# Kernel optimization log

Hardware: AMD Instinct MI355X
Metric: run time of the kernel (lower is better)

## Reference

```python
import jax, jax.numpy as jnp
import numpy as np

H = 8  # heads

def setup_inputs() -> dict:
    key = jax.random.key(0)
    k0, k1, k2, k3 = jax.random.split(key, 4)
    B, L, D = 4, 1024, 512
    K = jax.random.normal(k0, (B, L, D), dtype=jnp.float32)
    Q = jax.random.normal(k1, (B, L, D), dtype=jnp.float32)
    V = jax.random.normal(k2, (B, L, D), dtype=jnp.float32)
    # realistic padding: each doc has a valid length in [L/2, L]
    lengths = jax.random.randint(k3, (B,), L // 2, L + 1)
    pos = jnp.arange(L)
    valid = pos[None, :] < lengths[:, None]          # [B, L]
    pad_mask = valid[:, :, None] & valid[:, None, :]  # [B, L, L]
    bx_packed = ~valid                                # [B, L] True where padded
    doc_sizes = lengths.astype(jnp.float32)[:, None]  # [B, 1]
    gamma = jnp.ones((H,), dtype=jnp.float32)   # LayerNorm(heads) weight
    beta = jnp.zeros((H,), dtype=jnp.float32)   # LayerNorm(heads) bias
    return {"K": K, "Q": Q, "V": V, "doc_sizes": doc_sizes,
            "gamma": gamma, "beta": beta,
            "pad_mask": pad_mask, "bx_packed": bx_packed}


def reference(K, Q, V, doc_sizes, gamma, beta, pad_mask, bx_packed):
    B, L, D = K.shape
    d = D // H
    split = lambda x: x.reshape(B, L, H, d).transpose(0, 2, 1, 3)  # [B,H,L,d]
    k, q, v = split(K), split(Q), split(V)

    # InnerMatrix: inner-product similarity -> [B,H,L,L]
    cw = jnp.einsum('bhld,bhmd->bhlm', k, q)

    # LayerNorm over heads axis (torch views [B,H,L*L] -> [B,L*L,H], LN over H)
    mu = cw.mean(axis=1, keepdims=True)
    var = cw.var(axis=1, keepdims=True)
    cw = (cw - mu) / jnp.sqrt(var + 1e-5)
    cw = cw * gamma[None, :, None, None] + beta[None, :, None, None]
    # leaky = -1.0 default: float(leaky > 0) == 0, leaky-relu branch is a no-op

    # masked softmax over keys, NaN (fully-masked rows) -> 0
    cw = jnp.where(pad_mask[:, None, :, :], cw, -jnp.inf)
    cw = jax.nn.softmax(cw, axis=-1)
    cw = jnp.where(jnp.isnan(cw), 0.0, cw)

    # aggregated per-token weights: sum over queries, mean over heads -> [B,L]
    w = cw.sum(axis=-2).mean(axis=1)
    w = w / doc_sizes
    w = jnp.where(bx_packed, -jnp.inf, w)
    w = jax.nn.softmax(w, axis=-1)
    w = jnp.where(jnp.isnan(w), 0.0, w)

    # weighted V aggregation, merge heads back -> [B,L,D]
    out = jnp.einsum('bhlm,bhmd->bhld', cw, v)
    out = out.transpose(0, 2, 1, 3).reshape(B, L, D)
    return out, w[..., None]
```

## Files before the change

### kernel.cpp

```cpp
#include <hip/hip_runtime.h>
#include <math.h>

#define L_ 1024
#define D_ 512

typedef _Float16 half8 __attribute__((ext_vector_type(8)));
typedef _Float16 half4v __attribute__((ext_vector_type(4)));
typedef float floatx4 __attribute__((ext_vector_type(4)));

__global__ __launch_bounds__(256) void prep(
    const float* __restrict__ K, const float* __restrict__ Q,
    const float* __restrict__ V,
    _Float16* __restrict__ K16, _Float16* __restrict__ Q16,
    _Float16* __restrict__ Vt)
{
    __shared__ _Float16 tile[64][72];
    const int t = threadIdx.x;
    const int bi = blockIdx.x;
    if (bi < 256) {
        for (int it = 0; it < 16; ++it) {
            size_t f = (size_t)bi * 4096 + it * 256 + t;
            const float4* src; _Float16* dst;
            if (f < 524288) { src = (const float4*)K; dst = K16; }
            else            { src = (const float4*)Q; dst = Q16; f -= 524288; }
            float4 v = src[f];
            half4v h = { (_Float16)v.x, (_Float16)v.y, (_Float16)v.z, (_Float16)v.w };
            *(half4v*)&dst[f * 4] = h;
        }
    } else {
        const int id = bi - 256;
        const int mt = id & 15, h = (id >> 4) & 7, b = id >> 7;
        const float4* Vf4 = (const float4*)V;
        for (int it = 0; it < 4; ++it) {
            const int ml = (t >> 4) + 16 * it;
            const int c4 = t & 15;
            float4 v = Vf4[(size_t)(b * 1024 + mt * 64 + ml) * 128 + h * 16 + c4];
            tile[c4 * 4 + 0][ml] = (_Float16)v.x;
            tile[c4 * 4 + 1][ml] = (_Float16)v.y;
            tile[c4 * 4 + 2][ml] = (_Float16)v.z;
            tile[c4 * 4 + 3][ml] = (_Float16)v.w;
        }
        __syncthreads();
        const int d = t >> 2, seg = t & 3;
        half8 o0 = *(half8*)&tile[d][seg * 16];
        half8 o1 = *(half8*)&tile[d][seg * 16 + 8];
        size_t obase = ((size_t)(b * 8 + h) * 64 + d) * 1024 + mt * 64 + seg * 16;
        *(half8*)&Vt[obase] = o0;
        *(half8*)&Vt[obase + 8] = o1;
    }
}

__global__ __launch_bounds__(256) void qk_ln(
    const _Float16* __restrict__ K16, const _Float16* __restrict__ Q16,
    const float* __restrict__ gamma, const float* __restrict__ beta,
    _Float16* __restrict__ S)
{
    const int t = threadIdx.x;
    const int bi = blockIdx.x;
    const int b = bi & 3;
    const int lt = (bi >> 2) & 63;
    const int ms = bi >> 8;
    const int wv = t >> 6, lane = t & 63;
    const int col = lane & 15, quad = lane >> 4;

    const _Float16* Kb = K16 + (size_t)b * 524288;
    const _Float16* Qb = Q16 + (size_t)b * 524288;
    const size_t krow = (size_t)(lt * 16 + col) * 512;

    float g[8], be[8];
    #pragma unroll
    for (int h = 0; h < 8; ++h) { g[h] = gamma[h]; be[h] = beta[h]; }

    for (int i = 0; i < 4; ++i) {
        const int m0 = (ms * 16 + wv * 4 + i) * 16;
        const size_t qrow = (size_t)(m0 + col) * 512;
        floatx4 c[8];
        #pragma unroll
        for (int h = 0; h < 8; ++h) {
            half8 a0 = *(const half8*)&Kb[krow + h * 64 + quad * 8];
            half8 a1 = *(const half8*)&Kb[krow + h * 64 + 32 + quad * 8];
            half8 b0 = *(const half8*)&Qb[qrow + h * 64 + quad * 8];
            half8 b1 = *(const half8*)&Qb[qrow + h * 64 + 32 + quad * 8];
            floatx4 z = {0.f, 0.f, 0.f, 0.f};
            z    = __builtin_amdgcn_mfma_f32_16x16x32_f16(a0, b0, z, 0, 0, 0);
            c[h] = __builtin_amdgcn_mfma_f32_16x16x32_f16(a1, b1, z, 0, 0, 0);
        }
        #pragma unroll
        for (int r = 0; r < 4; ++r) {
            float mu = 0.f;
            #pragma unroll
            for (int h = 0; h < 8; ++h) mu += c[h][r];
            mu *= 0.125f;
            float var = 0.f;
            #pragma unroll
            for (int h = 0; h < 8; ++h) { float dd = c[h][r] - mu; var += dd * dd; }
            var *= 0.125f;
            const float rs = 1.0f / sqrtf(var + 1e-5f);
            const int l = lt * 16 + quad * 4 + r;
            #pragma unroll
            for (int h = 0; h < 8; ++h) {
                float val = (c[h][r] - mu) * rs * g[h] + be[h];
                S[((size_t)(b * 8 + h) * 1024 + l) * 1024 + m0 + col] = (_Float16)val;
            }
        }
    }
}

__global__ __launch_bounds__(256) void softmax_w(
    _Float16* __restrict__ S, const float* __restrict__ doc,
    float* __restrict__ wacc)
{
    __shared__ float cs[4][1024];
    const int t = threadIdx.x, wv = t >> 6, lane = t & 63;
    const int bi = blockIdx.x;
    const int b = bi & 3, lg = bi >> 2;
    const int len = (int)doc[b];

    float csum[16];
    #pragma unroll
    for (int j = 0; j < 16; ++j) csum[j] = 0.f;

    for (int k = 0; k < 16; ++k) {
        const int rr = wv * 16 + k;
        const int h = rr & 7, li = rr >> 3;
        const int l = lg * 8 + li;
        const size_t base = ((size_t)(b * 8 + h) * 1024 + l) * 1024;
        if (l >= len) {
            half8 z = {};
            *(half8*)&S[base + lane * 8] = z;
            *(half8*)&S[base + 512 + lane * 8] = z;
            continue;
        }
        half8 v1 = *(const half8*)&S[base + lane * 8];
        half8 v2 = *(const half8*)&S[base + 512 + lane * 8];
        float f1[8], f2[8];
        float mx = -INFINITY;
        #pragma unroll
        for (int j = 0; j < 8; ++j) { f1[j] = (float)v1[j]; mx = fmaxf(mx, f1[j]); }
        #pragma unroll
        for (int j = 0; j < 8; ++j) {
            const int m = 512 + lane * 8 + j;
            f2[j] = (m < len) ? (float)v2[j] : -INFINITY;
            mx = fmaxf(mx, f2[j]);
        }
        #pragma unroll
        for (int o = 1; o < 64; o <<= 1) mx = fmaxf(mx, __shfl_xor(mx, o));
        float e1[8], e2[8], sm = 0.f;
        #pragma unroll
        for (int j = 0; j < 8; ++j) { e1[j] = __expf(f1[j] - mx); sm += e1[j]; }
        #pragma unroll
        for (int j = 0; j < 8; ++j) {
            const int m = 512 + lane * 8 + j;
            e2[j] = (m < len) ? __expf(f2[j] - mx) : 0.f;
            sm += e2[j];
        }
        #pragma unroll
        for (int o = 1; o < 64; o <<= 1) sm += __shfl_xor(sm, o);
        const float inv = 1.0f / sm;
        half8 p1, p2;
        #pragma unroll
        for (int j = 0; j < 8; ++j) {
            float q1 = e1[j] * inv, q2 = e2[j] * inv;
            p1[j] = (_Float16)q1; p2[j] = (_Float16)q2;
            csum[j] += q1; csum[8 + j] += q2;
        }
        *(half8*)&S[base + lane * 8] = p1;
        *(half8*)&S[base + 512 + lane * 8] = p2;
    }
    #pragma unroll
    for (int j = 0; j < 8; ++j) {
        cs[wv][lane * 8 + j] = csum[j];
        cs[wv][512 + lane * 8 + j] = csum[8 + j];
    }
    __syncthreads();
    #pragma unroll
    for (int q = 0; q < 4; ++q) {
        const int mm = t + q * 256;
        float s = cs[0][mm] + cs[1][mm] + cs[2][mm] + cs[3][mm];
        atomicAdd(&wacc[b * 1024 + mm], s);
    }
}

__global__ __launch_bounds__(256) void pv(
    const _Float16* __restrict__ P, const _Float16* __restrict__ Vt,
    float* __restrict__ out)
{
    const int t = threadIdx.x, wv = t >> 6, lane = t & 63;
    const int col = lane & 15, quad = lane >> 4;
    const int bi = blockIdx.x;
    const int lb = bi & 15, h = (bi >> 4) & 7, b = bi >> 7;
    const int l0 = lb * 64 + wv * 16;
    const _Float16* Arow = P + ((size_t)(b * 8 + h) * 1024 + l0 + col) * 1024;
    const _Float16* Vb = Vt + (size_t)(b * 8 + h) * 65536;
    floatx4 acc[4] = {{0,0,0,0},{0,0,0,0},{0,0,0,0},{0,0,0,0}};
    for (int kc = 0; kc < 32; ++kc) {
        const int m0 = kc * 32 + quad * 8;
        half8 a = *(const half8*)&Arow[m0];
        #pragma unroll
        for (int dt = 0; dt < 4; ++dt) {
            half8 bf = *(const half8*)&Vb[(size_t)(dt * 16 + col) * 1024 + m0];
            acc[dt] = __builtin_amdgcn_mfma_f32_16x16x32_f16(a, bf, acc[dt], 0, 0, 0);
        }
    }
    #pragma unroll
    for (int r = 0; r < 4; ++r) {
        const int l = l0 + quad * 4 + r;
        float* orow = out + (size_t)(b * 1024 + l) * 512 + h * 64;
        #pragma unroll
        for (int dt = 0; dt < 4; ++dt)
            orow[dt * 16 + col] = acc[dt][r];
    }
}

__global__ __launch_bounds__(256) void w_final(
    const float* __restrict__ wacc, const float* __restrict__ doc,
    float* __restrict__ wout)
{
    const int b = blockIdx.x;
    const int t = threadIdx.x;
    __shared__ float red[4];

    const float ds = doc[b];
    const int len = (int)ds;

    float v[4];
    float mx = -INFINITY;
    #pragma unroll
    for (int i = 0; i < 4; ++i) {
        const int m = t + 256 * i;
        const float raw = wacc[b * L_ + m];
        v[i] = (m < len) ? (raw * 0.125f) / ds : -INFINITY;
        mx = fmaxf(mx, v[i]);
    }
    #pragma unroll
    for (int off = 1; off < 64; off <<= 1) mx = fmaxf(mx, __shfl_xor(mx, off));
    if ((t & 63) == 0) red[t >> 6] = mx;
    __syncthreads();
    mx = fmaxf(fmaxf(red[0], red[1]), fmaxf(red[2], red[3]));

    float e[4];
    float sm = 0.f;
    #pragma unroll
    for (int i = 0; i < 4; ++i) {
        e[i] = (v[i] != -INFINITY) ? __expf(v[i] - mx) : 0.f;
        sm += e[i];
    }
    #pragma unroll
    for (int off = 1; off < 64; off <<= 1) sm += __shfl_xor(sm, off);
    __syncthreads();
    if ((t & 63) == 0) red[t >> 6] = sm;
    __syncthreads();
    sm = red[0] + red[1] + red[2] + red[3];
    const float inv = (sm > 0.f) ? 1.0f / sm : 0.f;

    #pragma unroll
    for (int i = 0; i < 4; ++i)
        wout[b * L_ + t + 256 * i] = e[i] * inv;
}

extern "C" void kernel_launch(void* const* d_in, const int* in_sizes, int n_in,
                              void* d_out, int out_size, void* d_ws, size_t ws_size,
                              hipStream_t stream)
{
    const float* K     = (const float*)d_in[0];
    const float* Q     = (const float*)d_in[1];
    const float* V     = (const float*)d_in[2];
    const float* doc   = (const float*)d_in[3];
    const float* gamma = (const float*)d_in[4];
    const float* beta  = (const float*)d_in[5];

    float* out  = (float*)d_out;
    float* wout = out + (size_t)4 * L_ * D_;

    _Float16* S   = (_Float16*)d_ws;
    _Float16* K16 = S + (size_t)33554432;
    _Float16* Q16 = K16 + 2097152;
    _Float16* Vt  = Q16 + 2097152;
    float*    wacc = (float*)(Vt + 2097152);

    hipMemsetAsync(wacc, 0, 4096 * sizeof(float), stream);
    prep     <<<dim3(768),  dim3(256), 0, stream>>>(K, Q, V, K16, Q16, Vt);
    qk_ln    <<<dim3(1024), dim3(256), 0, stream>>>(K16, Q16, gamma, beta, S);
    softmax_w<<<dim3(512),  dim3(256), 0, stream>>>(S, doc, wacc);
    pv       <<<dim3(512),  dim3(256), 0, stream>>>(S, Vt, out);
    w_final  <<<dim3(4),    dim3(256), 0, stream>>>(wacc, doc, wout);
}
```

Before: 207.9 us.

## Fuse softmax exponent into QK kernel using fixed LayerNorm bound, normalize in PV

```diff
diff --git a/kernel.cpp b/kernel.cpp
--- a/kernel.cpp
+++ b/kernel.cpp
@@ -6,7 +6,10 @@
 
 typedef _Float16 half8 __attribute__((ext_vector_type(8)));
 typedef _Float16 half4v __attribute__((ext_vector_type(4)));
+typedef _Float16 half2v __attribute__((ext_vector_type(2)));
 typedef float floatx4 __attribute__((ext_vector_type(4)));
+
+#define LDS_PITCH 264
 
 __global__ __launch_bounds__(256) void prep(
     const float* __restrict__ K, const float* __restrict__ Q,
@@ -53,40 +56,61 @@
 __global__ __launch_bounds__(256) void qk_ln(
     const _Float16* __restrict__ K16, const _Float16* __restrict__ Q16,
     const float* __restrict__ gamma, const float* __restrict__ beta,
-    _Float16* __restrict__ S)
-{
-    const int t = threadIdx.x;
+    const float* __restrict__ doc,
+    _Float16* __restrict__ S, float* __restrict__ spart)
+{
+    __shared__ _Float16 se[8 * 16 * LDS_PITCH];
+
+    const int t  = threadIdx.x;
     const int bi = blockIdx.x;
-    const int b = bi & 3;
+    const int b  = bi & 3;
     const int lt = (bi >> 2) & 63;
-    const int ms = bi >> 8;
+    const int q  = bi >> 8;
     const int wv = t >> 6, lane = t & 63;
     const int col = lane & 15, quad = lane >> 4;
+    const int len = (int)doc[b];
+    const int lbase = lt * 16;
+
+    float g[8], be[8], M = 0.f;
+    #pragma unroll
+    for (int h = 0; h < 8; ++h) {
+        g[h] = gamma[h]; be[h] = beta[h];
+        M = fmaxf(M, 2.8285f * fabsf(g[h]) + fabsf(be[h]));
+    }
 
     const _Float16* Kb = K16 + (size_t)b * 524288;
     const _Float16* Qb = Q16 + (size_t)b * 524288;
-    const size_t krow = (size_t)(lt * 16 + col) * 512;
-
-    float g[8], be[8];
-    #pragma unroll
-    for (int h = 0; h < 8; ++h) { g[h] = gamma[h]; be[h] = beta[h]; }
-
-    for (int i = 0; i < 4; ++i) {
-        const int m0 = (ms * 16 + wv * 4 + i) * 16;
+    const size_t krow = (size_t)(lbase + col) * 512;
+
+    half8 a0[8], a1[8];
+    #pragma unroll
+    for (int h = 0; h < 8; ++h) {
+        a0[h] = *(const half8*)&Kb[krow + h * 64 + quad * 8];
+        a1[h] = *(const half8*)&Kb[krow + h * 64 + 32 + quad * 8];
+    }
+
+    float sum[8][4];
+    #pragma unroll
+    for (int h = 0; h < 8; ++h)
+        #pragma unroll
+        for (int r = 0; r < 4; ++r) sum[h][r] = 0.f;
+
+    for (int mt = 0; mt < 4; ++mt) {
+        const int m0 = q * 256 + wv * 64 + mt * 16;
         const size_t qrow = (size_t)(m0 + col) * 512;
         floatx4 c[8];
         #pragma unroll
         for (int h = 0; h < 8; ++h) {
-            half8 a0 = *(const half8*)&Kb[krow + h * 64 + quad * 8];
-            half8 a1 = *(const half8*)&Kb[krow + h * 64 + 32 + quad * 8];
             half8 b0 = *(const half8*)&Qb[qrow + h * 64 + quad * 8];
             half8 b1 = *(const half8*)&Qb[qrow + h * 64 + 32 + quad * 8];
             floatx4 z = {0.f, 0.f, 0.f, 0.f};
-            z    = __builtin_amdgcn_mfma_f32_16x16x32_f16(a0, b0, z, 0, 0, 0);
-            c[h] = __builtin_amdgcn_mfma_f32_16x16x32_f16(a1, b1, z, 0, 0, 0);
-        }
+            z    = __builtin_amdgcn_mfma_f32_16x16x32_f16(a0[h], b0, z, 0, 0, 0);
+            c[h] = __builtin_amdgcn_mfma_f32_16x16x32_f16(a1[h], b1, c[h] = z, 0, 0, 0);
+        }
+        const bool mok = (m0 + col) < len;
         #pragma unroll
         for (int r = 0; r < 4; ++r) {
+            const int l = lbase + quad * 4 + r;
             float mu = 0.f;
             #pragma unroll
             for (int h = 0; h < 8; ++h) mu += c[h][r];
@@ -96,106 +120,109 @@
             for (int h = 0; h < 8; ++h) { float dd = c[h][r] - mu; var += dd * dd; }
             var *= 0.125f;
             const float rs = 1.0f / sqrtf(var + 1e-5f);
-            const int l = lt * 16 + quad * 4 + r;
+            const bool keep = mok && (l < len);
             #pragma unroll
             for (int h = 0; h < 8; ++h) {
-                float val = (c[h][r] - mu) * rs * g[h] + be[h];
-                S[((size_t)(b * 8 + h) * 1024 + l) * 1024 + m0 + col] = (_Float16)val;
+                float e = 0.f;
+                if (keep) {
+                    float val = (c[h][r] - mu) * rs * g[h] + be[h];
+                    e = __expf(val - M);
+                }
+                sum[h][r] += e;
+                se[(h * 16 + quad * 4 + r) * LDS_PITCH + wv * 64 + mt * 16 + col] =
+                    (_Float16)e;
             }
         }
     }
-}
-
-__global__ __launch_bounds__(256) void softmax_w(
-    _Float16* __restrict__ S, const float* __restrict__ doc,
-    float* __restrict__ wacc)
-{
-    __shared__ float cs[4][1024];
-    const int t = threadIdx.x, wv = t >> 6, lane = t & 63;
-    const int bi = blockIdx.x;
-    const int b = bi & 3, lg = bi >> 2;
+
+    #pragma unroll
+    for (int h = 0; h < 8; ++h)
+        #pragma unroll
+        for (int r = 0; r < 4; ++r) {
+            float s = sum[h][r];
+            s += __shfl_xor(s, 1); s += __shfl_xor(s, 2);
+            s += __shfl_xor(s, 4); s += __shfl_xor(s, 8);
+            sum[h][r] = s;
+        }
+    if (col == 0) {
+        #pragma unroll
+        for (int h = 0; h < 8; ++h)
+            #pragma unroll
+            for (int r = 0; r < 4; ++r)
+                spart[((size_t)((b * 8 + h) * 1024 + lbase + quad * 4 + r)) * 16
+                      + q * 4 + wv] = sum[h][r];
+    }
+    __syncthreads();
+
+    for (int it = 0; it < 16; ++it) {
+        const int rr = it * 8 + (t >> 5);
+        const int h = rr >> 4, l = rr & 15;
+        half8 v = *(half8*)&se[rr * LDS_PITCH + (t & 31) * 8];
+        *(half8*)&S[((size_t)((b * 8 + h) * 1024 + lbase + l)) * 1024
+                    + q * 256 + (t & 31) * 8] = v;
+    }
+}
+
+__global__ __launch_bounds__(256) void stats_reduce(
+    const float* __restrict__ spart, const float* __restrict__ doc,
+    float* __restrict__ inv)
+{
+    const int i = blockIdx.x * 256 + threadIdx.x;
+    const int l = i & 1023;
+    const int b = i >> 13;
     const int len = (int)doc[b];
-
-    float csum[16];
-    #pragma unroll
-    for (int j = 0; j < 16; ++j) csum[j] = 0.f;
-
-    for (int k = 0; k < 16; ++k) {
-        const int rr = wv * 16 + k;
-        const int h = rr & 7, li = rr >> 3;
-        const int l = lg * 8 + li;
-        const size_t base = ((size_t)(b * 8 + h) * 1024 + l) * 1024;
-        if (l >= len) {
-            half8 z = {};
-            *(half8*)&S[base + lane * 8] = z;
-            *(half8*)&S[base + 512 + lane * 8] = z;
-            continue;
-        }
-        half8 v1 = *(const half8*)&S[base + lane * 8];
-        half8 v2 = *(const half8*)&S[base + 512 + lane * 8];
-        float f1[8], f2[8];
-        float mx = -INFINITY;
-        #pragma unroll
-        for (int j = 0; j < 8; ++j) { f1[j] = (float)v1[j]; mx = fmaxf(mx, f1[j]); }
-        #pragma unroll
-        for (int j = 0; j < 8; ++j) {
-            const int m = 512 + lane * 8 + j;
-            f2[j] = (m < len) ? (float)v2[j] : -INFINITY;
-            mx = fmaxf(mx, f2[j]);
-        }
-        #pragma unroll
-        for (int o = 1; o < 64; o <<= 1) mx = fmaxf(mx, __shfl_xor(mx, o));
-        float e1[8], e2[8], sm = 0.f;
-        #pragma unroll
-        for (int j = 0; j < 8; ++j) { e1[j] = __expf(f1[j] - mx); sm += e1[j]; }
-        #pragma unroll
-        for (int j = 0; j < 8; ++j) {
-            const int m = 512 + lane * 8 + j;
-            e2[j] = (m < len) ? __expf(f2[j] - mx) : 0.f;
-            sm += e2[j];
-        }
-        #pragma unroll
-        for (int o = 1; o < 64; o <<= 1) sm += __shfl_xor(sm, o);
-        const float inv = 1.0f / sm;
-        half8 p1, p2;
-        #pragma unroll
-        for (int j = 0; j < 8; ++j) {
-            float q1 = e1[j] * inv, q2 = e2[j] * inv;
-            p1[j] = (_Float16)q1; p2[j] = (_Float16)q2;
-            csum[j] += q1; csum[8 + j] += q2;
-        }
-        *(half8*)&S[base + lane * 8] = p1;
-        *(half8*)&S[base + 512 + lane * 8] = p2;
-    }
-    #pragma unroll
-    for (int j = 0; j < 8; ++j) {
-        cs[wv][lane * 8 + j] = csum[j];
-        cs[wv][512 + lane * 8 + j] = csum[8 + j];
-    }
-    __syncthreads();
-    #pragma unroll
-    for (int q = 0; q < 4; ++q) {
-        const int mm = t + q * 256;
-        float s = cs[0][mm] + cs[1][mm] + cs[2][mm] + cs[3][mm];
-        atomicAdd(&wacc[b * 1024 + mm], s);
-    }
+    float s = 0.f;
+    #pragma unroll
+    for (int j = 0; j < 16; ++j) s += spart[(size_t)i * 16 + j];
+    inv[i] = (l < len && s > 0.f) ? 1.0f / s : 0.f;
 }
 
 __global__ __launch_bounds__(256) void pv(
-    const _Float16* __restrict__ P, const _Float16* __restrict__ Vt,
-    float* __restrict__ out)
-{
+    const _Float16* __restrict__ S, const _Float16* __restrict__ Vt,
+    const float* __restrict__ invp,
+    float* __restrict__ out, float* __restrict__ wacc)
+{
+    __shared__ float cs[1024];
     const int t = threadIdx.x, wv = t >> 6, lane = t & 63;
     const int col = lane & 15, quad = lane >> 4;
     const int bi = blockIdx.x;
     const int lb = bi & 15, h = (bi >> 4) & 7, b = bi >> 7;
     const int l0 = lb * 64 + wv * 16;
-    const _Float16* Arow = P + ((size_t)(b * 8 + h) * 1024 + l0 + col) * 1024;
+
+    #pragma unroll
+    for (int i = 0; i < 4; ++i) cs[t + 256 * i] = 0.f;
+    __syncthreads();
+
+    const _Float16* Arow = S + ((size_t)(b * 8 + h) * 1024 + l0 + col) * 1024;
     const _Float16* Vb = Vt + (size_t)(b * 8 + h) * 65536;
+    const float inv = invp[(size_t)(b * 8 + h) * 1024 + l0 + col];
+
     floatx4 acc[4] = {{0,0,0,0},{0,0,0,0},{0,0,0,0},{0,0,0,0}};
     for (int kc = 0; kc < 32; ++kc) {
         const int m0 = kc * 32 + quad * 8;
-        half8 a = *(const half8*)&Arow[m0];
+        half8 e = *(const half8*)&Arow[m0];
+        half8 a;
+        #pragma unroll
+        for (int j = 0; j < 8; ++j) a[j] = (_Float16)((float)e[j] * inv);
+
+        #pragma unroll
+        for (int u = 0; u < 4; ++u) {
+            half2v p2 = { a[2 * u], a[2 * u + 1] };
+            int bits = *(int*)&p2;
+            #pragma unroll
+            for (int o = 1; o < 16; o <<= 1) {
+                int ob = __shfl_xor(bits, o);
+                half2v po = *(half2v*)&ob;
+                half2v pc = *(half2v*)&bits;
+                pc[0] = pc[0] + po[0]; pc[1] = pc[1] + po[1];
+                bits = *(int*)&pc;
+            }
+            if (col == 0) {
+                half2v pc = *(half2v*)&bits;
+                atomicAdd(&cs[m0 + 2 * u],     (float)pc[0]);
+                atomicAdd(&cs[m0 + 2 * u + 1], (float)pc[1]);
+            }
+        }
         #pragma unroll
         for (int dt = 0; dt < 4; ++dt) {
             half8 bf = *(const half8*)&Vb[(size_t)(dt * 16 + col) * 1024 + m0];
@@ -209,6 +236,12 @@
         #pragma unroll
         for (int dt = 0; dt < 4; ++dt)
             orow[dt * 16 + col] = acc[dt][r];
+    }
+    __syncthreads();
+    #pragma unroll
+    for (int i = 0; i < 4; ++i) {
+        const int m = t + 256 * i;
+        atomicAdd(&wacc[b * 1024 + m], cs[m]);
     }
 }
 
@@ -272,16 +305,18 @@
     float* out  = (float*)d_out;
     float* wout = out + (size_t)4 * L_ * D_;
 
-    _Float16* S   = (_Float16*)d_ws;
-    _Float16* K16 = S + (size_t)33554432;
-    _Float16* Q16 = K16 + 2097152;
-    _Float16* Vt  = Q16 + 2097152;
-    float*    wacc = (float*)(Vt + 2097152);
+    _Float16* S    = (_Float16*)d_ws;
+    _Float16* K16  = S + (size_t)33554432;
+    _Float16* Q16  = K16 + 2097152;
+    _Float16* Vt   = Q16 + 2097152;
+    float*    spart = (float*)(Vt + 2097152);
+    float*    invp  = spart + 524288;
+    float*    wacc  = invp + 32768;
 
     hipMemsetAsync(wacc, 0, 4096 * sizeof(float), stream);
-    prep     <<<dim3(768),  dim3(256), 0, stream>>>(K, Q, V, K16, Q16, Vt);
-    qk_ln    <<<dim3(1024), dim3(256), 0, stream>>>(K16, Q16, gamma, beta, S);
-    softmax_w<<<dim3(512),  dim3(256), 0, stream>>>(S, doc, wacc);
-    pv       <<<dim3(512),  dim3(256), 0, stream>>>(S, Vt, out);
-    w_final  <<<dim3(4),    dim3(256), 0, stream>>>(wacc, doc, wout);
-}
+    prep        <<<dim3(768),  dim3(256), 0, stream>>>(K, Q, V, K16, Q16, Vt);
+    qk_ln       <<<dim3(1024), dim3(256), 0, stream>>>(K16, Q16, gamma, beta, doc, S, spart);
+    stats_reduce<<<dim3(128),  dim3(256), 0, stream>>>(spart, doc, invp);
+    pv          <<<dim3(512),  dim3(256), 0, stream>>>(S, Vt, invp, out, wacc);
+    w_final     <<<dim3(4),    dim3(256), 0, stream>>>(wacc, doc, wout);
+}
```

New measurement: 202.2 us. 1.03x faster.

## Fuse QK, head LayerNorm, softmax and PV into one flash-style kernel

Applied to the files above, without the earlier changes.

```diff
diff --git a/kernel.cpp b/kernel.cpp
--- a/kernel.cpp
+++ b/kernel.cpp
@@ -7,6 +7,7 @@
 typedef _Float16 half8 __attribute__((ext_vector_type(8)));
 typedef _Float16 half4v __attribute__((ext_vector_type(4)));
 typedef float floatx4 __attribute__((ext_vector_type(4)));
+typedef float floatx2 __attribute__((ext_vector_type(2)));
 
 __global__ __launch_bounds__(256) void prep(
     const float* __restrict__ K, const float* __restrict__ Q,
@@ -50,165 +51,178 @@
     }
 }
 
-__global__ __launch_bounds__(256) void qk_ln(
+__global__ __launch_bounds__(256, 1) void fused(
     const _Float16* __restrict__ K16, const _Float16* __restrict__ Q16,
-    const float* __restrict__ gamma, const float* __restrict__ beta,
-    _Float16* __restrict__ S)
+    const _Float16* __restrict__ Vt,  const float* __restrict__ doc,
+    const float* __restrict__ gamma,  const float* __restrict__ beta,
+    float* __restrict__ out, float* __restrict__ wacc)
 {
-    const int t = threadIdx.x;
-    const int bi = blockIdx.x;
-    const int b = bi & 3;
-    const int lt = (bi >> 2) & 63;
-    const int ms = bi >> 8;
-    const int wv = t >> 6, lane = t & 63;
-    const int col = lane & 15, quad = lane >> 4;
-
-    const _Float16* Kb = K16 + (size_t)b * 524288;
+    extern __shared__ unsigned char smem[];
+    unsigned char* e8  = smem;
+    float* accf = (float*)smem;
+    float* rsum = (float*)(smem + 132096);
+    float* invs = (float*)(smem + 134144);
+
+    const int t = threadIdx.x, wv = t >> 6, lane = t & 63;
+    const int c = lane & 15, q = lane >> 4;
+    const int b = blockIdx.x & 3, lt = blockIdx.x >> 2;
+    const int l0 = lt * 16;
+    const int len = (int)doc[b];
+
+    float g[8], be[8], M = 0.f;
+    #pragma unroll
+    for (int h = 0; h < 8; ++h) {
+        g[h] = gamma[h]; be[h] = beta[h];
+        M = fmaxf(M, 2.8285f * fabsf(g[h]) + fabsf(be[h]));
+    }
+
+    const _Float16* Kb = K16 + (size_t)b * 524288 + (size_t)(l0 + c) * 512;
+    half8 kf0[8], kf1[8];
+    #pragma unroll
+    for (int h = 0; h < 8; ++h) {
+        kf0[h] = *(const half8*)&Kb[h * 64 + q * 8];
+        kf1[h] = *(const half8*)&Kb[h * 64 + 32 + q * 8];
+    }
+
+    floatx4 acc[8][4];
+    #pragma unroll
+    for (int h = 0; h < 8; ++h)
+        #pragma unroll
+        for (int dt = 0; dt < 4; ++dt) acc[h][dt] = (floatx4){0.f, 0.f, 0.f, 0.f};
+    float racc[8];
+    #pragma unroll
+    for (int h = 0; h < 8; ++h) racc[h] = 0.f;
+
     const _Float16* Qb = Q16 + (size_t)b * 524288;
-    const size_t krow = (size_t)(lt * 16 + col) * 512;
-
-    float g[8], be[8];
-    #pragma unroll
-    for (int h = 0; h < 8; ++h) { g[h] = gamma[h]; be[h] = beta[h]; }
-
-    for (int i = 0; i < 4; ++i) {
-        const int m0 = (ms * 16 + wv * 4 + i) * 16;
-        const size_t qrow = (size_t)(m0 + col) * 512;
-        floatx4 c[8];
+    const _Float16* Vb = Vt + (size_t)b * 524288;
+    const bool lok = (l0 + c) < len;
+    const int mbase = wv * 256;
+
+    for (int mt = 0; mt < 16; ++mt) {
+        const int tb = mbase + mt * 16;
+        const _Float16* Qr = Qb + (size_t)(tb + c) * 512;
+        floatx4 cf[8];
         #pragma unroll
         for (int h = 0; h < 8; ++h) {
-            half8 a0 = *(const half8*)&Kb[krow + h * 64 + quad * 8];
-            half8 a1 = *(const half8*)&Kb[krow + h * 64 + 32 + quad * 8];
-            half8 b0 = *(const half8*)&Qb[qrow + h * 64 + quad * 8];
-            half8 b1 = *(const half8*)&Qb[qrow + h * 64 + 32 + quad * 8];
+            half8 a0 = *(const half8*)&Qr[h * 64 + q * 8];
+            half8 a1 = *(const half8*)&Qr[h * 64 + 32 + q * 8];
             floatx4 z = {0.f, 0.f, 0.f, 0.f};
-            z    = __builtin_amdgcn_mfma_f32_16x16x32_f16(a0, b0, z, 0, 0, 0);
-            c[h] = __builtin_amdgcn_mfma_f32_16x16x32_f16(a1, b1, z, 0, 0, 0);
+            z     = __builtin_amdgcn_mfma_f32_16x16x32_f16(a0, kf0[h], z, 0, 0, 0);
+            cf[h] = __builtin_amdgcn_mfma_f32_16x16x32_f16(a1, kf1[h], z, 0, 0, 0);
         }
         #pragma unroll
         for (int r = 0; r < 4; ++r) {
+            const int m = tb + q * 4 + r;
+            const bool keep = lok && (m < len);
             float mu = 0.f;
             #pragma unroll
-            for (int h = 0; h < 8; ++h) mu += c[h][r];
+            for (int h = 0; h < 8; ++h) mu += cf[h][r];
             mu *= 0.125f;
             float var = 0.f;
             #pragma unroll
-            for (int h = 0; h < 8; ++h) { float dd = c[h][r] - mu; var += dd * dd; }
+            for (int h = 0; h < 8; ++h) { float dd = cf[h][r] - mu; var += dd * dd; }
             var *= 0.125f;
             const float rs = 1.0f / sqrtf(var + 1e-5f);
-            const int l = lt * 16 + quad * 4 + r;
             #pragma unroll
             for (int h = 0; h < 8; ++h) {
-                float val = (c[h][r] - mu) * rs * g[h] + be[h];
-                S[((size_t)(b * 8 + h) * 1024 + l) * 1024 + m0 + col] = (_Float16)val;
+                float ev = 0.f;
+                if (keep) {
+                    float val = (cf[h][r] - mu) * rs * g[h] + be[h];
+                    ev = __expf(val - M);
+                }
+                cf[h][r] = ev;
+                racc[h] += ev;
             }
         }
-    }
-}
-
-__global__ __launch_bounds__(256) void softmax_w(
-    _Float16* __restrict__ S, const float* __restrict__ doc,
-    float* __restrict__ wacc)
-{
-    __shared__ float cs[4][1024];
-    const int t = threadIdx.x, wv = t >> 6, lane = t & 63;
-    const int bi = blockIdx.x;
-    const int b = bi & 3, lg = bi >> 2;
-    const int len = (int)doc[b];
-
-    float csum[16];
-    #pragma unroll
-    for (int j = 0; j < 16; ++j) csum[j] = 0.f;
-
-    for (int k = 0; k < 16; ++k) {
-        const int rr = wv * 16 + k;
-        const int h = rr & 7, li = rr >> 3;
-        const int l = lg * 8 + li;
-        const size_t base = ((size_t)(b * 8 + h) * 1024 + l) * 1024;
-        if (l >= len) {
-            half8 z = {};
-            *(half8*)&S[base + lane * 8] = z;
-            *(half8*)&S[base + 512 + lane * 8] = z;
-            continue;
-        }
-        half8 v1 = *(const half8*)&S[base + lane * 8];
-        half8 v2 = *(const half8*)&S[base + 512 + lane * 8];
-        float f1[8], f2[8];
-        float mx = -INFINITY;
-        #pragma unroll
-        for (int j = 0; j < 8; ++j) { f1[j] = (float)v1[j]; mx = fmaxf(mx, f1[j]); }
+        #pragma unroll
+        for (int r = 0; r < 4; ++r) {
+            const int m = tb + q * 4 + r;
+            int lo = __builtin_amdgcn_cvt_pk_fp8_f32(cf[0][r], cf[1][r], 0, false);
+            lo     = __builtin_amdgcn_cvt_pk_fp8_f32(cf[2][r], cf[3][r], lo, true);
+            int hi = __builtin_amdgcn_cvt_pk_fp8_f32(cf[4][r], cf[5][r], 0, false);
+            hi     = __builtin_amdgcn_cvt_pk_fp8_f32(cf[6][r], cf[7][r], hi, true);
+            *(int2*)(e8 + ((size_t)(c * 1024 + (m ^ c)) * 8)) = make_int2(lo, hi);
+        }
+        #pragma unroll
+        for (int h = 0; h < 8; ++h) {
+            half4v pa;
+            #pragma unroll
+            for (int j = 0; j < 4; ++j) pa[j] = (_Float16)cf[h][j];
+            #pragma unroll
+            for (int dt = 0; dt < 4; ++dt) {
+                const _Float16* vr = Vb + (size_t)(h * 64 + dt * 16 + c) * 1024
+                                        + tb + q * 4;
+                half4v vb4 = *(const half4v*)vr;
+                acc[h][dt] = __builtin_amdgcn_mfma_f32_16x16x16f16(
+                    pa, vb4, acc[h][dt], 0, 0, 0);
+            }
+        }
+    }
+
+    #pragma unroll
+    for (int h = 0; h < 8; ++h) {
+        float s = racc[h];
+        s += __shfl_xor(s, 16);
+        s += __shfl_xor(s, 32);
+        if (q == 0) rsum[wv * 128 + c * 8 + h] = s;
+    }
+    __syncthreads();
+    if (t < 128) {
+        const int ll = t >> 3;
+        float s = rsum[t] + rsum[128 + t] + rsum[256 + t] + rsum[384 + t];
+        invs[t] = ((l0 + ll) < len && s > 0.f) ? 1.0f / s : 0.f;
+    }
+    __syncthreads();
+
+    {
+        float wsum[4] = {0.f, 0.f, 0.f, 0.f};
+        for (int l = 0; l < 16; ++l) {
+            floatx4 iv0 = *(floatx4*)&invs[l * 8];
+            floatx4 iv1 = *(floatx4*)&invs[l * 8 + 4];
+            #pragma unroll
+            for (int u = 0; u < 4; ++u) {
+                const int m = t + 256 * u;
+                int2 v = *(int2*)(e8 + ((size_t)(l * 1024 + (m ^ l)) * 8));
+                floatx2 p01 = __builtin_amdgcn_cvt_pk_f32_fp8(v.x, false);
+                floatx2 p23 = __builtin_amdgcn_cvt_pk_f32_fp8(v.x, true);
+                floatx2 p45 = __builtin_amdgcn_cvt_pk_f32_fp8(v.y, false);
+                floatx2 p67 = __builtin_amdgcn_cvt_pk_f32_fp8(v.y, true);
+                wsum[u] += p01[0] * iv0[0] + p01[1] * iv0[1]
+                         + p23[0] * iv0[2] + p23[1] * iv0[3]
+                         + p45[0] * iv1[0] + p45[1] * iv1[1]
+                         + p67[0] * iv1[2] + p67[1] * iv1[3];
+            }
+        }
+        #pragma unroll
+        for (int u = 0; u < 4; ++u)
+            atomicAdd(&wacc[b * 1024 + t + 256 * u], wsum[u]);
+    }
+    __syncthreads();
+
+    #pragma unroll
+    for (int h = 0; h < 8; ++h)
+        #pragma unroll
+        for (int dt = 0; dt < 4; ++dt)
+            #pragma unroll
+            for (int r = 0; r < 4; ++r)
+                accf[(size_t)(wv * 16 + q * 4 + r) * 516 + h * 64 + dt * 16 + c]
+                    = acc[h][dt][r];
+    __syncthreads();
+
+    {
+        const int l = t >> 4, hd0 = (t & 15) * 32;
+        const int h = hd0 >> 6;
+        const float iv = invs[l * 8 + h];
+        float* orow = out + (size_t)(b * 1024 + l0 + l) * 512 + hd0;
         #pragma unroll
         for (int j = 0; j < 8; ++j) {
-            const int m = 512 + lane * 8 + j;
-            f2[j] = (m < len) ? (float)v2[j] : -INFINITY;
-            mx = fmaxf(mx, f2[j]);
-        }
-        #pragma unroll
-        for (int o = 1; o < 64; o <<= 1) mx = fmaxf(mx, __shfl_xor(mx, o));
-        float e1[8], e2[8], sm = 0.f;
-        #pragma unroll
-        for (int j = 0; j < 8; ++j) { e1[j] = __expf(f1[j] - mx); sm += e1[j]; }
-        #pragma unroll
-        for (int j = 0; j < 8; ++j) {
-            const int m = 512 + lane * 8 + j;
-            e2[j] = (m < len) ? __expf(f2[j] - mx) : 0.f;
-            sm += e2[j];
-        }
-        #pragma unroll
-        for (int o = 1; o < 64; o <<= 1) sm += __shfl_xor(sm, o);
-        const float inv = 1.0f / sm;
-        half8 p1, p2;
-        #pragma unroll
-        for (int j = 0; j < 8; ++j) {
-            float q1 = e1[j] * inv, q2 = e2[j] * inv;
-            p1[j] = (_Float16)q1; p2[j] = (_Float16)q2;
-            csum[j] += q1; csum[8 + j] += q2;
-        }
-        *(half8*)&S[base + lane * 8] = p1;
-        *(half8*)&S[base + 512 + lane * 8] = p2;
-    }
-    #pragma unroll
-    for (int j = 0; j < 8; ++j) {
-        cs[wv][lane * 8 + j] = csum[j];
-        cs[wv][512 + lane * 8 + j] = csum[8 + j];
-    }
-    __syncthreads();
-    #pragma unroll
-    for (int q = 0; q < 4; ++q) {
-        const int mm = t + q * 256;
-        float s = cs[0][mm] + cs[1][mm] + cs[2][mm] + cs[3][mm];
-        atomicAdd(&wacc[b * 1024 + mm], s);
-    }
-}
-
-__global__ __launch_bounds__(256) void pv(
-    const _Float16* __restrict__ P, const _Float16* __restrict__ Vt,
-    float* __restrict__ out)
-{
-    const int t = threadIdx.x, wv = t >> 6, lane = t & 63;
-    const int col = lane & 15, quad = lane >> 4;
-    const int bi = blockIdx.x;
-    const int lb = bi & 15, h = (bi >> 4) & 7, b = bi >> 7;
-    const int l0 = lb * 64 + wv * 16;
-    const _Float16* Arow = P + ((size_t)(b * 8 + h) * 1024 + l0 + col) * 1024;
-    const _Float16* Vb = Vt + (size_t)(b * 8 + h) * 65536;
-    floatx4 acc[4] = {{0,0,0,0},{0,0,0,0},{0,0,0,0},{0,0,0,0}};
-    for (int kc = 0; kc < 32; ++kc) {
-        const int m0 = kc * 32 + quad * 8;
-        half8 a = *(const half8*)&Arow[m0];
-        #pragma unroll
-        for (int dt = 0; dt < 4; ++dt) {
-            half8 bf = *(const half8*)&Vb[(size_t)(dt * 16 + col) * 1024 + m0];
-            acc[dt] = __builtin_amdgcn_mfma_f32_16x16x32_f16(a, bf, acc[dt], 0, 0, 0);
-        }
-    }
-    #pragma unroll
-    for (int r = 0; r < 4; ++r) {
-        const int l = l0 + quad * 4 + r;
-        float* orow = out + (size_t)(b * 1024 + l) * 512 + h * 64;
-        #pragma unroll
-        for (int dt = 0; dt < 4; ++dt)
-            orow[dt * 16 + col] = acc[dt][r];
+            floatx4 s = {0.f, 0.f, 0.f, 0.f};
+            #pragma unroll
+            for (int w = 0; w < 4; ++w)
+                s += *(floatx4*)&accf[(size_t)(w * 16 + l) * 516 + hd0 + j * 4];
+            s *= iv;
+            *(floatx4*)&orow[j * 4] = s;
+        }
     }
 }
 
@@ -272,16 +286,17 @@
     float* out  = (float*)d_out;
     float* wout = out + (size_t)4 * L_ * D_;
 
-    _Float16* S   = (_Float16*)d_ws;
-    _Float16* K16 = S + (size_t)33554432;
+    _Float16* K16 = (_Float16*)d_ws;
     _Float16* Q16 = K16 + 2097152;
     _Float16* Vt  = Q16 + 2097152;
     float*    wacc = (float*)(Vt + 2097152);
 
-    hipMemsetAsync(wacc, 0, 4096 * sizeof(float), stream);
-    prep     <<<dim3(768),  dim3(256), 0, stream>>>(K, Q, V, K16, Q16, Vt);
-    qk_ln    <<<dim3(1024), dim3(256), 0, stream>>>(K16, Q16, gamma, beta, S);
-    softmax_w<<<dim3(512),  dim3(256), 0, stream>>>(S, doc, wacc);
-    pv       <<<dim3(512),  dim3(256), 0, stream>>>(S, Vt, out);
-    w_final  <<<dim3(4),    dim3(256), 0, stream>>>(wacc, doc, wout);
+    (void)hipFuncSetAttribute((const void*)fused,
+                              hipFuncAttributeMaxDynamicSharedMemorySize, 134656);
+
+    (void)hipMemsetAsync(wacc, 0, 4096 * sizeof(float), stream);
+    prep   <<<dim3(768), dim3(256), 0,      stream>>>(K, Q, V, K16, Q16, Vt);
+    fused  <<<dim3(256), dim3(256), 134656, stream>>>(K16, Q16, Vt, doc, gamma,
+                                                      beta, out, wacc);
+    w_final<<<dim3(4),   dim3(256), 0,      stream>>>(wacc, doc, wout);
 }
```

Measured after the change: 256.7 us. 1.23x slower.
